# Kernel optimization log

Hardware: AMD Instinct MI355X
Metric: run time of the kernel (lower is better)

The kernel has to match this reference:

```python
import jax, jax.numpy as jnp
import numpy as np

HEADS = 4
NDECAY = 4


def setup_inputs() -> dict:
    key = jax.random.key(0)
    ks = jax.random.split(key, 6)
    B, C, T = 4, 192, 2048
    s = 1.0 / np.sqrt(C)
    return {
        "x": jax.random.normal(ks[0], (B, C, T), dtype=jnp.float32),
        "Wq": jax.random.normal(ks[1], (C, C), dtype=jnp.float32) * s,
        "bq": jnp.zeros((C,), dtype=jnp.float32),
        "Wk": jax.random.normal(ks[2], (C, C), dtype=jnp.float32) * s,
        "bk": jnp.zeros((C,), dtype=jnp.float32),
        "Wc": jax.random.normal(ks[3], (C, C), dtype=jnp.float32) * s,
        "bc": jnp.zeros((C,), dtype=jnp.float32),
        "Wd": jax.random.normal(ks[4], (C, HEADS * NDECAY), dtype=jnp.float32) * s,
        "bd": jnp.zeros((HEADS * NDECAY,), dtype=jnp.float32),
        "Wp": jax.random.normal(ks[5], (C, C), dtype=jnp.float32) * s,
        "bp": jnp.zeros((C,), dtype=jnp.float32),
    }


def reference(x, Wq, bq, Wk, bk, Wc, bc, Wd, bd, Wp, bp):
    B, C, T = x.shape
    heads, ndecay = HEADS, NDECAY
    hd = C // heads
    xt = jnp.transpose(x, (0, 2, 1))  # (B, T, C)

    def split_heads(y):  # (B, T, D) -> (B, heads, D//heads, T)
        return jnp.transpose(y, (0, 2, 1)).reshape(B, heads, -1, T)

    queries = split_heads(xt @ Wq + bq)   # (B, h, hd, T)
    keys = split_heads(xt @ Wk + bk)      # (B, h, hd, T)
    content = split_heads(xt @ Wc + bc)   # (B, h, hd, T)

    # dots[b,h,t,s] = <keys[...,t], queries[...,s]> / sqrt(hd)
    dots = jnp.einsum('bhct,bhcs->bhts', keys, queries) / jnp.sqrt(
        jnp.asarray(hd, x.dtype))

    # learned decay bias
    decay_q = split_heads(xt @ Wd + bd)                 # (B, h, ndecay, T)
    decay_q = jax.nn.sigmoid(decay_q) / 2
    delta = (jnp.arange(T, dtype=x.dtype)[:, None]
             - jnp.arange(T, dtype=x.dtype)[None, :])   # (T, T)
    decays = jnp.arange(1, ndecay + 1, dtype=x.dtype)
    decay_kernel = -decays.reshape(-1, 1, 1) * jnp.abs(delta) / jnp.sqrt(
        jnp.asarray(ndecay, x.dtype))                   # (ndecay, T, T)
    dots = dots + jnp.einsum('fts,bhfs->bhts', decay_kernel, decay_q)

    # mask diagonal
    idx = jnp.arange(T)
    dots = dots.at[..., idx, idx].set(-100)

    weights = jax.nn.softmax(dots, axis=2)              # softmax over t (keys)
    result = jnp.einsum('bhts,bhct->bhcs', weights, content).reshape(B, C, T)

    out = jnp.transpose(result, (0, 2, 1)) @ Wp + bp + xt  # (B, T, C)
    return jnp.transpose(out, (0, 2, 1))                    # (B, C, T)
```

## Files before the change

kernel.cpp:

```cpp
#include <hip/hip_runtime.h>

typedef __attribute__((ext_vector_type(8))) short short8;
typedef __attribute__((ext_vector_type(4))) float f32x4;

constexpr int Bn = 4, Cn = 192, Tn = 2048, Hn = 4, HD = 48;
constexpr float LOG2E = 1.4426950408889634f;
constexpr float QK_SCALE2 = 0.14433756729740643f * 1.4426950408889634f;
constexpr float NEG100_LOG2 = -100.0f * 1.4426950408889634f;

__device__ inline unsigned short f2bf(float f) {
  unsigned int u = __builtin_bit_cast(unsigned int, f);
  return (unsigned short)((u + 0x7FFFu + ((u >> 16) & 1u)) >> 16);
}
__device__ inline float bf2f(unsigned short h) {
  unsigned int u = ((unsigned int)h) << 16;
  return __builtin_bit_cast(float, u);
}
__device__ inline f32x4 mfma16(short8 a, short8 b, f32x4 c) {
  return __builtin_amdgcn_mfma_f32_16x16x32_bf16(a, b, c, 0, 0, 0);
}
__device__ inline unsigned int cvtpk(float lo, float hi) {
  unsigned int r;
  asm("v_cvt_pk_bf16_f32 %0, %1, %2" : "=v"(r) : "v"(lo), "v"(hi));
  return r;
}

__global__ __launch_bounds__(256) void transpose_xw(const float* __restrict__ x,
                                                    const float* __restrict__ Wq,
                                                    const float* __restrict__ Wk,
                                                    const float* __restrict__ Wc,
                                                    const float* __restrict__ Wp,
                                                    short* __restrict__ xt,
                                                    short* __restrict__ WT) {
  __shared__ short tile[32][40];
  int tid = threadIdx.x;
  int row = tid >> 3, q = tid & 7;
  int z = blockIdx.z;
  if (z < Bn) {
    int t0 = blockIdx.x * 32, c0 = blockIdx.y * 32, b = z;
    float4 v = *(const float4*)(x + ((size_t)(b * Cn + c0 + row)) * Tn + t0 + q * 4);
    tile[row][q * 4 + 0] = (short)f2bf(v.x);
    tile[row][q * 4 + 1] = (short)f2bf(v.y);
    tile[row][q * 4 + 2] = (short)f2bf(v.z);
    tile[row][q * 4 + 3] = (short)f2bf(v.w);
    __syncthreads();
    ushort4 pk;
    pk.x = (unsigned short)tile[q * 4 + 0][row];
    pk.y = (unsigned short)tile[q * 4 + 1][row];
    pk.z = (unsigned short)tile[q * 4 + 2][row];
    pk.w = (unsigned short)tile[q * 4 + 3][row];
    *(ushort4*)(xt + ((size_t)(b * Tn + t0 + row)) * Cn + c0 + q * 4) = pk;
  } else {
    int idx = blockIdx.y * 64 + blockIdx.x;
    if (idx >= 144) return;
    int j = idx / 36, t = idx - j * 36;
    int k0 = (t / 6) * 32, n0 = (t % 6) * 32;
    const float* W = (j == 0) ? Wq : (j == 1) ? Wk : (j == 2) ? Wc : Wp;
    float4 v = *(const float4*)(W + (size_t)(k0 + row) * Cn + n0 + q * 4);
    tile[row][q * 4 + 0] = (short)f2bf(v.x);
    tile[row][q * 4 + 1] = (short)f2bf(v.y);
    tile[row][q * 4 + 2] = (short)f2bf(v.z);
    tile[row][q * 4 + 3] = (short)f2bf(v.w);
    __syncthreads();
    ushort4 pk;
    pk.x = (unsigned short)tile[q * 4 + 0][row];
    pk.y = (unsigned short)tile[q * 4 + 1][row];
    pk.z = (unsigned short)tile[q * 4 + 2][row];
    pk.w = (unsigned short)tile[q * 4 + 3][row];
    *(ushort4*)(WT + ((size_t)(j * Cn + n0 + row)) * Cn + k0 + q * 4) = pk;
  }
}

__global__ __launch_bounds__(256) void gemm_qkv(const short* __restrict__ WT,
                                                const float* __restrict__ bq,
                                                const float* __restrict__ bk,
                                                const float* __restrict__ bc,
                                                const short* __restrict__ Bsrc,
                                                short* __restrict__ Qt,
                                                short* __restrict__ Kt,
                                                short* __restrict__ Vc) {
  constexpr int LDK = 200;
  __shared__ short As[64 * LDK];
  __shared__ short Bs[128 * LDK];
  int tt = blockIdx.x, nt = blockIdx.y, b = blockIdx.z;
  int j = nt / 3;
  int ln0 = (nt - j * 3) * 64;
  int n0g = nt * 64;
  int t0 = tt * 128;
  const float* bias = (j == 0) ? bq : (j == 1) ? bk : bc;
  int tid = threadIdx.x, w = tid >> 6, l = tid & 63;
  int g16 = l >> 4, c16 = l & 15;

  for (int idx = tid; idx < 4608; idx += 256) {
    if (idx < 1536) {
      int row = idx / 24, ch = idx % 24;
      *(float4*)(&As[row * LDK + ch * 8]) =
          *(const float4*)(WT + ((size_t)(n0g + row)) * Cn + ch * 8);
    } else {
      int jj = idx - 1536;
      int row = jj / 24, ch = jj % 24;
      *(float4*)(&Bs[row * LDK + ch * 8]) =
          *(const float4*)(Bsrc + ((size_t)(b * Tn + t0 + row)) * Cn + ch * 8);
    }
  }
  __syncthreads();

  f32x4 acc[4][2];
#pragma unroll
  for (int m = 0; m < 4; ++m)
#pragma unroll
    for (int n = 0; n < 2; ++n) acc[m][n] = (f32x4){0.f, 0.f, 0.f, 0.f};

#pragma unroll
  for (int kk = 0; kk < 6; ++kk) {
    short8 af[4], bf[2];
#pragma unroll
    for (int m = 0; m < 4; ++m)
      af[m] = *(const short8*)(&As[(m * 16 + c16) * LDK + kk * 32 + g16 * 8]);
#pragma unroll
    for (int n = 0; n < 2; ++n)
      bf[n] = *(const short8*)(&Bs[(w * 32 + n * 16 + c16) * LDK + kk * 32 + g16 * 8]);
#pragma unroll
    for (int m = 0; m < 4; ++m)
#pragma unroll
      for (int n = 0; n < 2; ++n) acc[m][n] = mfma16(af[m], bf[n], acc[m][n]);
  }

#pragma unroll
  for (int m = 0; m < 4; ++m)
#pragma unroll
    for (int n = 0; n < 2; ++n) {
      int nrow = ln0 + m * 16 + g16 * 4;
      int tcol = t0 + w * 32 + n * 16 + c16;
      if (j == 2) {
#pragma unroll
        for (int r = 0; r < 4; ++r)
          Vc[((size_t)(b * Cn + nrow + r)) * Tn + tcol] =
              (short)f2bf(acc[m][n][r] + bias[nrow + r]);
      } else {
        short* O = j ? Kt : Qt;
        ushort4 pk;
        pk.x = f2bf(acc[m][n][0] + bias[nrow + 0]);
        pk.y = f2bf(acc[m][n][1] + bias[nrow + 1]);
        pk.z = f2bf(acc[m][n][2] + bias[nrow + 2]);
        pk.w = f2bf(acc[m][n][3] + bias[nrow + 3]);
        *(ushort4*)(O + ((size_t)(b * Tn + tcol)) * Cn + nrow) = pk;
      }
    }
}

__global__ __launch_bounds__(256) void decay_g(const short* __restrict__ xt,
                                               const float* __restrict__ Wd,
                                               const float* __restrict__ bd,
                                               float* __restrict__ gout) {
  int idx = blockIdx.x * 256 + threadIdx.x;
  int kq = idx & 7;
  int t = (idx >> 3) & 2047;
  int b = idx >> 14;
  const short* xr = xt + ((size_t)(b * Tn + t)) * Cn + kq * 24;
  const float* wr = Wd + kq * 24 * 16;
  float d[16];
#pragma unroll
  for (int n = 0; n < 16; ++n) d[n] = 0.f;
#pragma unroll
  for (int k = 0; k < 24; k += 8) {
    short8 xv8 = *(const short8*)(xr + k);
#pragma unroll
    for (int jj = 0; jj < 8; ++jj) {
      float xv = bf2f((unsigned short)xv8[jj]);
      const float* wrow = wr + (k + jj) * 16;
#pragma unroll
      for (int n = 0; n < 16; ++n) d[n] = fmaf(xv, wrow[n], d[n]);
    }
  }
#pragma unroll
  for (int n = 0; n < 16; ++n) {
    d[n] += __shfl_xor(d[n], 1);
    d[n] += __shfl_xor(d[n], 2);
    d[n] += __shfl_xor(d[n], 4);
  }
  if (kq == 0) {
#pragma unroll
    for (int h = 0; h < 4; ++h) {
      float gsum = 0.f;
#pragma unroll
      for (int f = 0; f < 4; ++f) {
        float s = 1.f / (1.f + __expf(-(d[h * 4 + f] + bd[h * 4 + f])));
        gsum += (float)(f + 1) * s;
      }
      gout[((size_t)(b * 4 + h)) * Tn + t] = 0.25f * gsum;
    }
  }
}

__global__ __launch_bounds__(512, 4) void attn(const short* __restrict__ Qt,
                                               const short* __restrict__ Kt,
                                               const short* __restrict__ Vc,
                                               const float* __restrict__ gbuf,
                                               unsigned short* __restrict__ Pacc,
                                               float* __restrict__ Plsum,
                                               int kchunk) {
  __shared__ short Kb[2][64][64];
  __shared__ short Vb[2][48][64];
  __shared__ short Pl[8][16][64];
  const int s0 = blockIdx.x * 128;
  const int bh = blockIdx.y;
  const int b = bh >> 2, h = bh & 3;
  const int ks = blockIdx.z;
  const int tid = threadIdx.x, w = tid >> 6, l = tid & 63;
  const int g16 = l >> 4, c16 = l & 15;
  const int sx = c16 & 7;
  const int tstart = ks * kchunk, tend = tstart + kchunk;

  const short* Kbase = Kt + (size_t)b * Tn * Cn + h * HD;
  const short* Vbase = Vc + ((size_t)(b * Cn + h * HD)) * Tn;

  float4 z4;
  z4.x = z4.y = z4.z = z4.w = 0.f;
  if (tid < 256) {
    int bufz = tid >> 7, r = (tid >> 1) & 63, chp = 6 + (tid & 1);
    *(float4*)(&Kb[bufz][r][(chp ^ (r & 7)) * 8]) = z4;
  }
  for (int idx = tid; idx < 768; idx += 512) {
    int row = idx / 6, ch = idx % 6;
    *(float4*)(&Kb[row >> 6][row & 63][(ch ^ (row & 7)) * 8]) =
        *(const float4*)(Qt + ((size_t)(b * Tn + s0 + row)) * Cn + h * HD + ch * 8);
  }
  __syncthreads();
  short8 qf[2];
  {
    int qr = (w & 3) * 16 + c16, qb_ = w >> 2;
    qf[0] = *(const short8*)(&Kb[qb_][qr][(g16 ^ sx) * 8]);
    qf[1] = *(const short8*)(&Kb[qb_][qr][((4 + g16) ^ sx) * 8]);
  }
  __syncthreads();

  for (int idx = tid; idx < 768; idx += 512) {
    if (idx < 384) {
      int row = idx / 6, ch = idx % 6;
      *(float4*)(&Kb[0][row][(ch ^ (row & 7)) * 8]) =
          *(const float4*)(Kbase + ((size_t)(tstart + row)) * Cn + ch * 8);
    } else {
      int jj = idx - 384, row = jj >> 3, ch = jj & 7;
      *(float4*)(&Vb[0][row][(ch ^ (row & 7)) * 8]) =
          *(const float4*)(Vbase + (size_t)row * Tn + tstart + ch * 8);
    }
  }
  __syncthreads();

  const bool aIsK = tid < 384;
  const int arow = aIsK ? tid / 6 : ((tid - 384) >> 3);
  const int ach = aIsK ? tid % 6 : ((tid - 384) & 7);
  const int dA = arow * 64 + ((ach ^ (arow & 7)) * 8);
  const bool hasB = tid < 256;
  const int brow = (128 + tid) >> 3, bch = (128 + tid) & 7;
  const int dB = brow * 64 + ((bch ^ (brow & 7)) * 8);

  const int s_lane = s0 + w * 16 + c16;
  const int sref = s0 + ((w >> 2) << 6);
  const float g2 = gbuf[((size_t)(b * 4 + h)) * Tn + s_lane] * LOG2E;
  const float g16x = g2 * 16.0f;
  const float rb1 = g2, rb2 = g2 * 2.0f, rb3 = g2 * 3.0f;
  float base = g2 * (float)(tstart + g16 * 4 - s_lane);
  const float binc = g2 * 64.0f;
  float lsum = 0.f;
  f32x4 acc[3];
#pragma unroll
  for (int cs = 0; cs < 3; ++cs) acc[cs] = (f32x4){0.f, 0.f, 0.f, 0.f};

  int buf = 0;
  for (int t0 = tstart; t0 < tend; t0 += 64) {
    const int tn = t0 + 64;
    const bool hn = tn < tend;
    float4 r0, r1;
    if (hn) {
      r0 = aIsK ? *(const float4*)(Kbase + (size_t)(tn + arow) * Cn + ach * 8)
                : *(const float4*)(Vbase + (size_t)arow * Tn + tn + ach * 8);
      if (hasB) r1 = *(const float4*)(Vbase + (size_t)brow * Tn + tn + bch * 8);
    }
    const short* KbP = &Kb[buf][0][0];
    const short* VbP = &Vb[buf][0][0];

    f32x4 sacc[4];
#pragma unroll
    for (int m = 0; m < 4; ++m) sacc[m] = (f32x4){0.f, 0.f, 0.f, 0.f};
    __builtin_amdgcn_s_setprio(1);
#pragma unroll
    for (int kk = 0; kk < 2; ++kk)
#pragma unroll
      for (int m = 0; m < 4; ++m) {
        short8 af = *(const short8*)(KbP + (m * 16 + c16) * 64 + (((kk * 4 + g16) ^ sx) * 8));
        sacc[m] = mfma16(af, qf[kk], sacc[m]);
      }
    __builtin_amdgcn_s_setprio(0);

    if (t0 > sref) {
      float nbm = -base;
#pragma unroll
      for (int m = 0; m < 4; ++m) {
        float e0 = __builtin_amdgcn_exp2f(fmaf(sacc[m][0], QK_SCALE2, nbm));
        float e1 = __builtin_amdgcn_exp2f(fmaf(sacc[m][1], QK_SCALE2, nbm) - rb1);
        float e2 = __builtin_amdgcn_exp2f(fmaf(sacc[m][2], QK_SCALE2, nbm) - rb2);
        float e3 = __builtin_amdgcn_exp2f(fmaf(sacc[m][3], QK_SCALE2, nbm) - rb3);
        lsum += (e0 + e1) + (e2 + e3);
        unsigned long long u64v =
            ((unsigned long long)cvtpk(e2, e3) << 32) | (unsigned long long)cvtpk(e0, e1);
        *(unsigned long long*)(&Pl[w][c16][(((2 * m + (g16 >> 1)) ^ sx) * 8) + (g16 & 1) * 4]) =
            u64v;
        nbm -= g16x;
      }
    } else if (t0 < sref) {
      float pbm = base;
#pragma unroll
      for (int m = 0; m < 4; ++m) {
        float e0 = __builtin_amdgcn_exp2f(fmaf(sacc[m][0], QK_SCALE2, pbm));
        float e1 = __builtin_amdgcn_exp2f(fmaf(sacc[m][1], QK_SCALE2, pbm) + rb1);
        float e2 = __builtin_amdgcn_exp2f(fmaf(sacc[m][2], QK_SCALE2, pbm) + rb2);
        float e3 = __builtin_amdgcn_exp2f(fmaf(sacc[m][3], QK_SCALE2, pbm) + rb3);
        lsum += (e0 + e1) + (e2 + e3);
        unsigned long long u64v =
            ((unsigned long long)cvtpk(e2, e3) << 32) | (unsigned long long)cvtpk(e0, e1);
        *(unsigned long long*)(&Pl[w][c16][(((2 * m + (g16 >> 1)) ^ sx) * 8) + (g16 & 1) * 4]) =
            u64v;
        pbm += g16x;
      }
    } else {
      const float fbd = (float)(t0 + g16 * 4 - s_lane);
#pragma unroll
      for (int m = 0; m < 4; ++m) {
        float e[4];
#pragma unroll
        for (int r = 0; r < 4; ++r) {
          float d = fbd + (float)(16 * m + r);
          float ad = fabsf(d);
          float v = fmaf(-g2, ad, sacc[m][r] * QK_SCALE2);
          v = (ad < 0.5f) ? NEG100_LOG2 : v;
          e[r] = __builtin_amdgcn_exp2f(v);
        }
        lsum += (e[0] + e[1]) + (e[2] + e[3]);
        unsigned long long u64v = ((unsigned long long)cvtpk(e[2], e[3]) << 32) |
                                  (unsigned long long)cvtpk(e[0], e[1]);
        *(unsigned long long*)(&Pl[w][c16][(((2 * m + (g16 >> 1)) ^ sx) * 8) + (g16 & 1) * 4]) =
            u64v;
      }
    }
    base += binc;
    asm volatile("s_waitcnt lgkmcnt(0)" ::: "memory");

    __builtin_amdgcn_s_setprio(1);
#pragma unroll
    for (int kk = 0; kk < 2; ++kk) {
      short8 pf = *(const short8*)(&Pl[w][c16][((kk * 4 + g16) ^ sx) * 8]);
#pragma unroll
      for (int cs = 0; cs < 3; ++cs) {
        short8 vf = *(const short8*)(VbP + (cs * 16 + c16) * 64 + (((kk * 4 + g16) ^ sx) * 8));
        acc[cs] = mfma16(vf, pf, acc[cs]);
      }
    }
    __builtin_amdgcn_s_setprio(0);
    __syncthreads();
    if (hn) {
      short* KbN = &Kb[buf ^ 1][0][0];
      short* VbN = &Vb[buf ^ 1][0][0];
      if (aIsK)
        *(float4*)(KbN + dA) = r0;
      else
        *(float4*)(VbN + dA) = r0;
      if (hasB) *(float4*)(VbN + dB) = r1;
    }
    __syncthreads();
    buf ^= 1;
  }

  float lsum2 = lsum + __shfl_xor(lsum, 16);
  lsum2 += __shfl_xor(lsum2, 32);
  if (g16 == 0) Plsum[((size_t)(ks * 16 + bh)) * Tn + s_lane] = lsum2;

  unsigned int* Ob = (unsigned int*)&Kb[0][0][0];
  const int orow = w * 16 + c16;
#pragma unroll
  for (int cs = 0; cs < 3; ++cs) {
    Ob[orow * 24 + cs * 8 + g16 * 2 + 0] = cvtpk(acc[cs][0], acc[cs][1]);
    Ob[orow * 24 + cs * 8 + g16 * 2 + 1] = cvtpk(acc[cs][2], acc[cs][3]);
  }
  __syncthreads();
  float4* dst = (float4*)(Pacc + (((size_t)(ks * 16 + bh)) * Tn + s0) * 48);
  const float4* src = (const float4*)Ob;
  dst[tid] = src[tid];
  if (tid < 256) dst[tid + 512] = src[tid + 512];
}

__global__ __launch_bounds__(256) void combine(const unsigned short* __restrict__ Pacc,
                                               const float* __restrict__ Plsum,
                                               short* __restrict__ Rt, int KS) {
  int idx = blockIdx.x * 256 + threadIdx.x;
  int c4 = idx % 48;
  int rest = idx / 48;
  int s = rest & 2047;
  int b = rest >> 11;
  int c = c4 * 4;
  int h = c / 48;
  int cc = c - h * 48;
  size_t qb = ((size_t)(b * 4 + h)) * Tn + s;
  float a0 = 0.f, a1 = 0.f, a2 = 0.f, a3 = 0.f, lt = 0.f;
  for (int ks = 0; ks < KS; ++ks) {
    ushort4 v = *(const ushort4*)(Pacc + ((size_t)ks * 16 * Tn + qb) * 48 + cc);
    a0 += bf2f(v.x);
    a1 += bf2f(v.y);
    a2 += bf2f(v.z);
    a3 += bf2f(v.w);
    lt += Plsum[(size_t)ks * 16 * Tn + qb];
  }
  float inv = 1.f / lt;
  ushort4 pk;
  pk.x = f2bf(a0 * inv);
  pk.y = f2bf(a1 * inv);
  pk.z = f2bf(a2 * inv);
  pk.w = f2bf(a3 * inv);
  *(ushort4*)(Rt + ((size_t)(b * Tn + s)) * Cn + c) = pk;
}

__global__ __launch_bounds__(256) void gemm_out(const short* __restrict__ Awt,
                                                const float* __restrict__ bias,
                                                const short* __restrict__ Bsrc,
                                                float* __restrict__ O,
                                                const float* __restrict__ Xres) {
  constexpr int LDK = 200;
  __shared__ short As[64 * LDK];
  __shared__ short Bs[64 * LDK];
  int tt = blockIdx.x, nt = blockIdx.y, b = blockIdx.z;
  int n0 = nt * 64, t0 = tt * 64;
  int tid = threadIdx.x, w = tid >> 6, l = tid & 63;
  int g16 = l >> 4, c16 = l & 15;

  for (int idx = tid; idx < 3072; idx += 256) {
    if (idx < 1536) {
      int row = idx / 24, ch = idx % 24;
      *(float4*)(&As[row * LDK + ch * 8]) =
          *(const float4*)(Awt + ((size_t)(n0 + row)) * Cn + ch * 8);
    } else {
      int j = idx - 1536;
      int row = j / 24, ch = j % 24;
      *(float4*)(&Bs[row * LDK + ch * 8]) =
          *(const float4*)(Bsrc + ((size_t)(b * Tn + t0 + row)) * Cn + ch * 8);
    }
  }
  __syncthreads();

  f32x4 acc[4];
#pragma unroll
  for (int m = 0; m < 4; ++m) acc[m] = (f32x4){0.f, 0.f, 0.f, 0.f};

#pragma unroll
  for (int kk = 0; kk < 6; ++kk) {
    short8 bf = *(const short8*)(&Bs[(w * 16 + c16) * LDK + kk * 32 + g16 * 8]);
#pragma unroll
    for (int m = 0; m < 4; ++m) {
      short8 af = *(const short8*)(&As[(m * 16 + c16) * LDK + kk * 32 + g16 * 8]);
      acc[m] = mfma16(af, bf, acc[m]);
    }
  }

#pragma unroll
  for (int m = 0; m < 4; ++m) {
    int nrow = n0 + m * 16 + g16 * 4;
    int tcol = t0 + w * 16 + c16;
#pragma unroll
    for (int r = 0; r < 4; ++r) {
      size_t i = ((size_t)(b * Cn + nrow + r)) * Tn + tcol;
      O[i] = acc[m][r] + bias[nrow + r] + Xres[i];
    }
  }
}

extern "C" void kernel_launch(void* const* d_in, const int* in_sizes, int n_in,
                              void* d_out, int out_size, void* d_ws, size_t ws_size,
                              hipStream_t stream) {
  const float* x = (const float*)d_in[0];
  const float* Wq = (const float*)d_in[1];
  const float* bq = (const float*)d_in[2];
  const float* Wk = (const float*)d_in[3];
  const float* bk = (const float*)d_in[4];
  const float* Wc = (const float*)d_in[5];
  const float* bc = (const float*)d_in[6];
  const float* Wd = (const float*)d_in[7];
  const float* bd = (const float*)d_in[8];
  const float* Wp = (const float*)d_in[9];
  const float* bp = (const float*)d_in[10];
  float* out = (float*)d_out;

  char* ws = (char*)d_ws;
  const size_t SZ = (size_t)Bn * Tn * Cn * sizeof(short);
  short* XTbf = (short*)(ws);
  short* Qt = (short*)(ws + SZ);
  short* Kt = (short*)(ws + 2 * SZ);
  short* Vc = (short*)(ws + 3 * SZ);
  short* Rt = (short*)(ws + 4 * SZ);
  short* WT = (short*)(ws + 5 * SZ);
  float* gbuf = (float*)(ws + 5 * SZ + 294912);
  char* pbase = ws + 5 * SZ + 294912 + 131072;

  const size_t base = 5 * SZ + 294912 + 131072;
  const size_t perks = (size_t)16 * Tn * 48 * 2 + (size_t)16 * Tn * 4;
  int KS = 2;
  if (ws_size && base + 2 * perks > ws_size) KS = 1;
  unsigned short* Pacc = (unsigned short*)pbase;
  float* Plsum = (float*)(pbase + (size_t)KS * 16 * Tn * 48 * 2);

  transpose_xw<<<dim3(Tn / 32, Cn / 32, Bn + 1), 256, 0, stream>>>(x, Wq, Wk, Wc, Wp,
                                                                   XTbf, WT);
  gemm_qkv<<<dim3(16, 9, Bn), 256, 0, stream>>>(WT, bq, bk, bc, XTbf, Qt, Kt, Vc);
  decay_g<<<dim3(256), 256, 0, stream>>>(XTbf, Wd, bd, gbuf);
  attn<<<dim3(Tn / 128, Bn * Hn, KS), 512, 0, stream>>>(Qt, Kt, Vc, gbuf, Pacc, Plsum,
                                                        Tn / KS);
  combine<<<dim3(Bn * Tn * 48 / 256), 256, 0, stream>>>(Pacc, Plsum, Rt, KS);
  gemm_out<<<dim3(32, 3, Bn), 256, 0, stream>>>(WT + 3 * 36864, bp, Rt, out, x);
}
```

Before: 76.87 us.

## Fuse split-K combine into attention via last-block atomic counter; drop a barrier

Removes the separate combine kernel. Each attention block increments a per-tile atomic counter, and the block that arrives last sums the partial outputs and softmax denominators from all K splits and writes the normalized bf16 result. This saves a kernel launch and a pass over the partial buffers. It also drops a __syncthreads before the next-buffer LDS stores, which risks a read/write race on the double buffers. The counter is never zeroed, so the design relies on parity (odd count means last) across repeated calls.

```diff
diff --git a/kernel.cpp b/kernel.cpp
--- a/kernel.cpp
+++ b/kernel.cpp
@@ -199,10 +199,13 @@
                                                const float* __restrict__ gbuf,
                                                unsigned short* __restrict__ Pacc,
                                                float* __restrict__ Plsum,
-                                               int kchunk) {
+                                               short* __restrict__ Rt,
+                                               unsigned int* __restrict__ cnt,
+                                               int kchunk, int KS) {
   __shared__ short Kb[2][64][64];
   __shared__ short Vb[2][48][64];
   __shared__ short Pl[8][16][64];
+  __shared__ unsigned int lastflag;
   const int s0 = blockIdx.x * 128;
   const int bh = blockIdx.y;
   const int b = bh >> 2, h = bh & 3;
@@ -358,7 +361,6 @@
       }
     }
     __builtin_amdgcn_s_setprio(0);
-    __syncthreads();
     if (hn) {
       short* KbN = &Kb[buf ^ 1][0][0];
       short* VbN = &Vb[buf ^ 1][0][0];
@@ -388,36 +390,40 @@
   const float4* src = (const float4*)Ob;
   dst[tid] = src[tid];
   if (tid < 256) dst[tid + 512] = src[tid + 512];
-}
-
-__global__ __launch_bounds__(256) void combine(const unsigned short* __restrict__ Pacc,
-                                               const float* __restrict__ Plsum,
-                                               short* __restrict__ Rt, int KS) {
-  int idx = blockIdx.x * 256 + threadIdx.x;
-  int c4 = idx % 48;
-  int rest = idx / 48;
-  int s = rest & 2047;
-  int b = rest >> 11;
-  int c = c4 * 4;
-  int h = c / 48;
-  int cc = c - h * 48;
-  size_t qb = ((size_t)(b * 4 + h)) * Tn + s;
-  float a0 = 0.f, a1 = 0.f, a2 = 0.f, a3 = 0.f, lt = 0.f;
-  for (int ks = 0; ks < KS; ++ks) {
-    ushort4 v = *(const ushort4*)(Pacc + ((size_t)ks * 16 * Tn + qb) * 48 + cc);
-    a0 += bf2f(v.x);
-    a1 += bf2f(v.y);
-    a2 += bf2f(v.z);
-    a3 += bf2f(v.w);
-    lt += Plsum[(size_t)ks * 16 * Tn + qb];
-  }
-  float inv = 1.f / lt;
-  ushort4 pk;
-  pk.x = f2bf(a0 * inv);
-  pk.y = f2bf(a1 * inv);
-  pk.z = f2bf(a2 * inv);
-  pk.w = f2bf(a3 * inv);
-  *(ushort4*)(Rt + ((size_t)(b * Tn + s)) * Cn + c) = pk;
+
+  __syncthreads();
+  if (tid == 0) {
+    __threadfence();
+    lastflag = atomicAdd(&cnt[blockIdx.x * 16 + bh], 1u);
+  }
+  __syncthreads();
+  unsigned int lf = lastflag;
+  bool is_last = (KS <= 1) || ((lf & 1u) == 1u);
+  if (!is_last) return;
+  __threadfence();
+
+  for (int o = tid; o < 1536; o += 512) {
+    int r = o / 12, cc4 = o - r * 12;
+    int s = s0 + r;
+    size_t qb = (size_t)bh * Tn + s;
+    float a0 = 0.f, a1 = 0.f, a2 = 0.f, a3 = 0.f, lt = 0.f;
+    for (int k2 = 0; k2 < KS; ++k2) {
+      const unsigned short* p = Pacc + ((size_t)k2 * 16 * Tn + qb) * 48 + cc4 * 4;
+      ushort4 v = *(const ushort4*)p;
+      a0 += bf2f(v.x);
+      a1 += bf2f(v.y);
+      a2 += bf2f(v.z);
+      a3 += bf2f(v.w);
+      lt += Plsum[(size_t)k2 * 16 * Tn + qb];
+    }
+    float inv = 1.f / lt;
+    ushort4 pk;
+    pk.x = f2bf(a0 * inv);
+    pk.y = f2bf(a1 * inv);
+    pk.z = f2bf(a2 * inv);
+    pk.w = f2bf(a3 * inv);
+    *(ushort4*)(Rt + ((size_t)(b * Tn + s)) * Cn + h * HD + cc4 * 4) = pk;
+  }
 }
 
 __global__ __launch_bounds__(256) void gemm_out(const short* __restrict__ Awt,
@@ -503,16 +509,16 @@
   const size_t base = 5 * SZ + 294912 + 131072;
   const size_t perks = (size_t)16 * Tn * 48 * 2 + (size_t)16 * Tn * 4;
   int KS = 2;
-  if (ws_size && base + 2 * perks > ws_size) KS = 1;
+  if (ws_size && base + 2 * perks + 1024 > ws_size) KS = 1;
   unsigned short* Pacc = (unsigned short*)pbase;
   float* Plsum = (float*)(pbase + (size_t)KS * 16 * Tn * 48 * 2);
+  unsigned int* cnt = (unsigned int*)(pbase + (size_t)KS * perks);
 
   transpose_xw<<<dim3(Tn / 32, Cn / 32, Bn + 1), 256, 0, stream>>>(x, Wq, Wk, Wc, Wp,
                                                                    XTbf, WT);
   gemm_qkv<<<dim3(16, 9, Bn), 256, 0, stream>>>(WT, bq, bk, bc, XTbf, Qt, Kt, Vc);
   decay_g<<<dim3(256), 256, 0, stream>>>(XTbf, Wd, bd, gbuf);
   attn<<<dim3(Tn / 128, Bn * Hn, KS), 512, 0, stream>>>(Qt, Kt, Vc, gbuf, Pacc, Plsum,
-                                                        Tn / KS);
-  combine<<<dim3(Bn * Tn * 48 / 256), 256, 0, stream>>>(Pacc, Plsum, Rt, KS);
+                                                        Rt, cnt, Tn / KS, KS);
   gemm_out<<<dim3(32, 3, Bn), 256, 0, stream>>>(WT + 3 * 36864, bp, Rt, out, x);
 }
```

Result: slower. 120.0 us (+56.1%).
